# Kernel tuning notes

Hardware: AMD Instinct MI355X
Metric: run time of the kernel (lower is better)

The kernel has to match this reference:

```python
import jax, jax.numpy as jnp
import numpy as np

LSH_BUCKETS = 32
LSH_BANDWIDTH = 2.0
N_HASHES = 4
K_MAX = 64


def setup_inputs() -> dict:
    key0 = jax.random.key(0)
    kq, kk, kw = jax.random.split(key0, 3)
    B, L, D = 4, 4096, 64
    query = jax.random.normal(kq, (B, L, D), dtype=jnp.float32)
    key = jax.random.normal(kk, (B, L, D), dtype=jnp.float32)
    # learned LSH projection: maps binary features (D) -> N_HASHES hash values
    W = jax.random.normal(kw, (D, N_HASHES), dtype=jnp.float32)
    return {"query": query, "key": key, "W": W, "head_idx": 0}


def _lsh_hash(x_bin, W):
    # standard E2LSH-style hash: floor(<x, w> / bandwidth) mod n_buckets
    proj = x_bin @ W  # (B, L, N_HASHES)
    return jnp.floor(proj / LSH_BANDWIDTH).astype(jnp.int32) % LSH_BUCKETS


def reference(query, key, W, head_idx):
    B, L, _ = query.shape
    # binary_quantize: (x > 0).float()
    q_bin = (query > 0).astype(query.dtype)
    k_bin = (key > 0).astype(key.dtype)
    qh = _lsh_hash(q_bin, W)  # (B, L, N_HASHES) ints in [0, LSH_BUCKETS)
    kh = _lsh_hash(k_bin, W)
    # pack the N_HASHES hash values into one integer code per token;
    # codes equal  <=>  all hash values equal (values are in [0, LSH_BUCKETS))
    radix = (LSH_BUCKETS ** jnp.arange(N_HASHES)).astype(jnp.int32)  # (N_HASHES,)
    q_code = jnp.sum(qh * radix, axis=-1)  # (B, L)
    k_code = jnp.sum(kh * radix, axis=-1)  # (B, L)
    # match[b, i, j] = all hashes of query i equal hashes of key j
    match = q_code[:, :, None] == k_code[:, None, :]  # (B, L, L) bool
    # collect first K_MAX matching j per (b, i), pad with -1 (matches the
    # sequential early-break loop since j is scanned in increasing order)
    j_idx = jnp.arange(L, dtype=jnp.int32)
    score = jnp.where(match, j_idx[None, None, :], L)  # non-matches pushed to end
    first = jnp.sort(score, axis=-1)[:, :, :K_MAX]      # (B, L, K_MAX)
    candidates = jnp.where(first < L, first, -1)        # int32 indices, -1 pad
    return candidates
```

## Files before the change

kernel.cpp:

```cpp
#include <hip/hip_runtime.h>

#define KMAX 64
#define BB 4
#define LL 4096
#define DD 64
#define TOK (BB * LL)

typedef unsigned long long u64;

__global__ __launch_bounds__(64) void codes_kernel(
        const float* __restrict__ q,
        const float* __restrict__ k,
        const float* __restrict__ W,
        int* __restrict__ codes ) {
    __shared__ float sW[DD * 4];
    int lane = threadIdx.x;
    #pragma unroll
    for (int i = 0; i < 4; ++i) sW[i * 64 + lane] = W[i * 64 + lane];
    __syncthreads();

    int u = blockIdx.x * 64 + lane;
    const float* src = (u < TOK) ? q : k;
    int t = u & (TOK - 1);

    const float4* xp = (const float4*)(src + (size_t)t * DD);
    float4 x[16];
    #pragma unroll
    for (int i = 0; i < 16; ++i) x[i] = xp[i];

    float p0 = 0.f, p1 = 0.f, p2 = 0.f, p3 = 0.f;
    const float4* wrow = (const float4*)sW;
    #pragma unroll
    for (int d = 0; d < DD; ++d) {
        float xv = ((const float*)x)[d];
        float b = (xv > 0.f) ? 1.0f : 0.0f;
        float4 w = wrow[d];
        p0 = fmaf(b, w.x, p0);
        p1 = fmaf(b, w.y, p1);
        p2 = fmaf(b, w.z, p2);
        p3 = fmaf(b, w.w, p3);
    }
    int h0 = ((int)floorf(p0 * 0.5f)) & 31;
    int h1 = ((int)floorf(p1 * 0.5f)) & 31;
    int h2 = ((int)floorf(p2 * 0.5f)) & 31;
    int h3 = ((int)floorf(p3 * 0.5f)) & 31;
    codes[u] = h0 | (h1 << 5) | (h2 << 10) | (h3 << 15);
}

__global__ __launch_bounds__(256) void find_kernel(
        const int* __restrict__ qcodes,
        const int* __restrict__ kcodes,
        int* __restrict__ out) {
    int gtid = blockIdx.x * 256 + threadIdx.x;
    int wave = gtid >> 6;
    int lane = gtid & 63;
    int b = wave >> 12;
    int qc = qcodes[wave];
    const int4* kc4 = (const int4*)(kcodes + b * LL);
    int* op = out + (size_t)wave * KMAX;
    u64 lowmask = (1ull << lane) - 1ull;

    int count = 0;
    for (int g = 0; g < LL / 256 && count < KMAX; ++g) {
        int4 kv = kc4[g * 64 + lane];
        bool m0 = (kv.x == qc), m1 = (kv.y == qc);
        bool m2 = (kv.z == qc), m3 = (kv.w == qc);
        if (__ballot(m0 | m1 | m2 | m3) == 0) continue;
        u64 b0 = __ballot(m0), b1 = __ballot(m1);
        u64 b2 = __ballot(m2), b3 = __ballot(m3);
        int before = __popcll(b0 & lowmask) + __popcll(b1 & lowmask)
                   + __popcll(b2 & lowmask) + __popcll(b3 & lowmask);
        int pos = count + before;
        int j0 = g * 256 + lane * 4;
        if (m0) { if (pos < KMAX) op[pos] = j0;     ++pos; }
        if (m1) { if (pos < KMAX) op[pos] = j0 + 1; ++pos; }
        if (m2) { if (pos < KMAX) op[pos] = j0 + 2; ++pos; }
        if (m3) { if (pos < KMAX) op[pos] = j0 + 3; ++pos; }
        count += __popcll(b0) + __popcll(b1) + __popcll(b2) + __popcll(b3);
    }
    int p = count + lane;
    if (p < KMAX) op[p] = -1;
}

extern "C" void kernel_launch(void* const* d_in, const int* in_sizes, int n_in,
                              void* d_out, int out_size, void* d_ws, size_t ws_size,
                              hipStream_t stream) {
    const float* q = (const float*)d_in[0];
    const float* k = (const float*)d_in[1];
    const float* W = (const float*)d_in[2];
    int* out = (int*)d_out;
    int* codes = (int*)d_ws;
    int* qcodes = codes;
    int* kcodes = codes + TOK;

    codes_kernel<<<(2 * TOK) / 64, 64, 0, stream>>>(q, k, W, codes);

    const int total_threads = TOK * 64;
    find_kernel<<<total_threads / 256, 256, 0, stream>>>(qcodes, kcodes, out);
}
```

Baseline: 23.69 us.

## Fuse code hashing and candidate search into one cooperative kernel

```diff
diff --git a/kernel.cpp b/kernel.cpp
--- a/kernel.cpp
+++ b/kernel.cpp
@@ -1,33 +1,119 @@
 #include <hip/hip_runtime.h>
+#include <hip/hip_cooperative_groups.h>
+
+namespace cg = cooperative_groups;
 
 #define KMAX 64
 #define BB 4
 #define LL 4096
 #define DD 64
 #define TOK (BB * LL)
+#define NBLK 512
+#define QPW 8
 
 typedef unsigned long long u64;
+
+__global__ __launch_bounds__(256) void fused_kernel(
+        const float* __restrict__ q,
+        const float* __restrict__ k,
+        const float* __restrict__ W,
+        int* __restrict__ codes ,
+        int* __restrict__ out) {
+    __shared__ float sW[DD * 4];
+    int tid = threadIdx.x;
+    sW[tid] = W[tid];
+    __syncthreads();
+
+    int gt = blockIdx.x * 256 + tid;
+
+    if (gt < 2 * TOK) {
+        const float* src = (gt < TOK) ? q : k;
+        int t = gt & (TOK - 1);
+        const float4* xp = (const float4*)(src + (size_t)t * DD);
+        float4 x[16];
+        #pragma unroll
+        for (int i = 0; i < 16; ++i) x[i] = xp[i];
+
+        float p0 = 0.f, p1 = 0.f, p2 = 0.f, p3 = 0.f;
+        const float4* wrow = (const float4*)sW;
+        #pragma unroll
+        for (int d = 0; d < DD; ++d) {
+            float xv = ((const float*)x)[d];
+            float b = (xv > 0.f) ? 1.0f : 0.0f;
+            float4 w = wrow[d];
+            p0 = fmaf(b, w.x, p0);
+            p1 = fmaf(b, w.y, p1);
+            p2 = fmaf(b, w.z, p2);
+            p3 = fmaf(b, w.w, p3);
+        }
+        int h0 = ((int)floorf(p0 * 0.5f)) & 31;
+        int h1 = ((int)floorf(p1 * 0.5f)) & 31;
+        int h2 = ((int)floorf(p2 * 0.5f)) & 31;
+        int h3 = ((int)floorf(p3 * 0.5f)) & 31;
+        codes[gt] = h0 | (h1 << 5) | (h2 << 10) | (h3 << 15);
+    }
+
+    cg::this_grid().sync();
+
+    int lane = tid & 63;
+    int wv = gt >> 6;
+    int qbase = wv * QPW;
+    int b = qbase >> 12;
+    const int4* kc4 = (const int4*)(codes + TOK + b * LL);
+    const int* qp = codes + qbase;
+    int* outb = out + (size_t)qbase * KMAX;
+    u64 lowmask = (1ull << lane) - 1ull;
+
+    int qc[QPW], cnt[QPW];
+    #pragma unroll
+    for (int i = 0; i < QPW; ++i) { qc[i] = qp[i]; cnt[i] = 0; }
+
+    for (int g = 0; g < LL / 256; ++g) {
+        int4 kv = kc4[g * 64 + lane];
+        int j0 = g * 256 + lane * 4;
+        #pragma unroll
+        for (int i = 0; i < QPW; ++i) {
+            if (cnt[i] >= KMAX) continue;
+            bool m0 = (kv.x == qc[i]), m1 = (kv.y == qc[i]);
+            bool m2 = (kv.z == qc[i]), m3 = (kv.w == qc[i]);
+            if (__ballot(m0 | m1 | m2 | m3) == 0) continue;
+            u64 b0 = __ballot(m0), b1 = __ballot(m1);
+            u64 b2 = __ballot(m2), b3 = __ballot(m3);
+            int before = __popcll(b0 & lowmask) + __popcll(b1 & lowmask)
+                       + __popcll(b2 & lowmask) + __popcll(b3 & lowmask);
+            int pos = cnt[i] + before;
+            int* op = outb + i * KMAX;
+            if (m0) { if (pos < KMAX) op[pos] = j0;     ++pos; }
+            if (m1) { if (pos < KMAX) op[pos] = j0 + 1; ++pos; }
+            if (m2) { if (pos < KMAX) op[pos] = j0 + 2; ++pos; }
+            if (m3) { if (pos < KMAX) op[pos] = j0 + 3; ++pos; }
+            cnt[i] += __popcll(b0) + __popcll(b1) + __popcll(b2) + __popcll(b3);
+        }
+    }
+    #pragma unroll
+    for (int i = 0; i < QPW; ++i) {
+        int p = cnt[i] + lane;
+        if (p < KMAX) outb[i * KMAX + p] = -1;
+    }
+}
 
 __global__ __launch_bounds__(64) void codes_kernel(
         const float* __restrict__ q,
         const float* __restrict__ k,
         const float* __restrict__ W,
-        int* __restrict__ codes ) {
+        int* __restrict__ codes) {
     __shared__ float sW[DD * 4];
     int lane = threadIdx.x;
     #pragma unroll
     for (int i = 0; i < 4; ++i) sW[i * 64 + lane] = W[i * 64 + lane];
     __syncthreads();
-
     int u = blockIdx.x * 64 + lane;
     const float* src = (u < TOK) ? q : k;
     int t = u & (TOK - 1);
-
     const float4* xp = (const float4*)(src + (size_t)t * DD);
     float4 x[16];
     #pragma unroll
     for (int i = 0; i < 16; ++i) x[i] = xp[i];
-
     float p0 = 0.f, p1 = 0.f, p2 = 0.f, p3 = 0.f;
     const float4* wrow = (const float4*)sW;
     #pragma unroll
@@ -59,7 +145,6 @@
     const int4* kc4 = (const int4*)(kcodes + b * LL);
     int* op = out + (size_t)wave * KMAX;
     u64 lowmask = (1ull << lane) - 1ull;
-
     int count = 0;
     for (int g = 0; g < LL / 256 && count < KMAX; ++g) {
         int4 kv = kc4[g * 64 + lane];
@@ -90,11 +175,13 @@
     const float* W = (const float*)d_in[2];
     int* out = (int*)d_out;
     int* codes = (int*)d_ws;
-    int* qcodes = codes;
-    int* kcodes = codes + TOK;
 
-    codes_kernel<<<(2 * TOK) / 64, 64, 0, stream>>>(q, k, W, codes);
-
-    const int total_threads = TOK * 64;
-    find_kernel<<<total_threads / 256, 256, 0, stream>>>(qcodes, kcodes, out);
+    void* args[] = {(void*)&q, (void*)&k, (void*)&W, (void*)&codes, (void*)&out};
+    hipError_t e = hipLaunchCooperativeKernel((const void*)fused_kernel,
+                                              dim3(NBLK), dim3(256), args, 0, stream);
+    if (e != hipSuccess) {
+        (void)hipGetLastError();
+        codes_kernel<<<(2 * TOK) / 64, 64, 0, stream>>>(q, k, W, codes);
+        find_kernel<<<(TOK * 64) / 256, 256, 0, stream>>>(codes, codes + TOK, out);
+    }
 }
```

After: 73.85 us. +211.7%, slower.

## Process four queries per wavefront to reuse key code loads

Applied to the files above, without the earlier changes.

```diff
diff --git a/kernel.cpp b/kernel.cpp
--- a/kernel.cpp
+++ b/kernel.cpp
@@ -5,6 +5,7 @@
 #define LL 4096
 #define DD 64
 #define TOK (BB * LL)
+#define QPW 4
 
 typedef unsigned long long u64;
 
@@ -54,32 +55,49 @@
     int gtid = blockIdx.x * 256 + threadIdx.x;
     int wave = gtid >> 6;
     int lane = gtid & 63;
-    int b = wave >> 12;
-    int qc = qcodes[wave];
+    int qbase = wave * QPW;
+    int b = qbase >> 12;
     const int4* kc4 = (const int4*)(kcodes + b * LL);
-    int* op = out + (size_t)wave * KMAX;
+    const int* qp = qcodes + qbase;
+    int* outb = out + (size_t)qbase * KMAX;
     u64 lowmask = (1ull << lane) - 1ull;
 
-    int count = 0;
-    for (int g = 0; g < LL / 256 && count < KMAX; ++g) {
+    int qc[QPW], cnt[QPW];
+    #pragma unroll
+    for (int i = 0; i < QPW; ++i) { qc[i] = qp[i]; cnt[i] = 0; }
+
+    for (int g = 0; g < LL / 256; ++g) {
         int4 kv = kc4[g * 64 + lane];
-        bool m0 = (kv.x == qc), m1 = (kv.y == qc);
-        bool m2 = (kv.z == qc), m3 = (kv.w == qc);
-        if (__ballot(m0 | m1 | m2 | m3) == 0) continue;
-        u64 b0 = __ballot(m0), b1 = __ballot(m1);
-        u64 b2 = __ballot(m2), b3 = __ballot(m3);
-        int before = __popcll(b0 & lowmask) + __popcll(b1 & lowmask)
-                   + __popcll(b2 & lowmask) + __popcll(b3 & lowmask);
-        int pos = count + before;
+        bool a0 = (kv.x == qc[0]) | (kv.y == qc[0]) | (kv.z == qc[0]) | (kv.w == qc[0]);
+        bool a1 = (kv.x == qc[1]) | (kv.y == qc[1]) | (kv.z == qc[1]) | (kv.w == qc[1]);
+        bool a2 = (kv.x == qc[2]) | (kv.y == qc[2]) | (kv.z == qc[2]) | (kv.w == qc[2]);
+        bool a3 = (kv.x == qc[3]) | (kv.y == qc[3]) | (kv.z == qc[3]) | (kv.w == qc[3]);
+        if (__ballot(a0 | a1 | a2 | a3) == 0) continue;
         int j0 = g * 256 + lane * 4;
-        if (m0) { if (pos < KMAX) op[pos] = j0;     ++pos; }
-        if (m1) { if (pos < KMAX) op[pos] = j0 + 1; ++pos; }
-        if (m2) { if (pos < KMAX) op[pos] = j0 + 2; ++pos; }
-        if (m3) { if (pos < KMAX) op[pos] = j0 + 3; ++pos; }
-        count += __popcll(b0) + __popcll(b1) + __popcll(b2) + __popcll(b3);
+        #pragma unroll
+        for (int i = 0; i < QPW; ++i) {
+            if (cnt[i] >= KMAX) continue;
+            bool m0 = (kv.x == qc[i]), m1 = (kv.y == qc[i]);
+            bool m2 = (kv.z == qc[i]), m3 = (kv.w == qc[i]);
+            if (__ballot(m0 | m1 | m2 | m3) == 0) continue;
+            u64 b0 = __ballot(m0), b1 = __ballot(m1);
+            u64 b2 = __ballot(m2), b3 = __ballot(m3);
+            int before = __popcll(b0 & lowmask) + __popcll(b1 & lowmask)
+                       + __popcll(b2 & lowmask) + __popcll(b3 & lowmask);
+            int pos = cnt[i] + before;
+            int* op = outb + i * KMAX;
+            if (m0) { if (pos < KMAX) op[pos] = j0;     ++pos; }
+            if (m1) { if (pos < KMAX) op[pos] = j0 + 1; ++pos; }
+            if (m2) { if (pos < KMAX) op[pos] = j0 + 2; ++pos; }
+            if (m3) { if (pos < KMAX) op[pos] = j0 + 3; ++pos; }
+            cnt[i] += __popcll(b0) + __popcll(b1) + __popcll(b2) + __popcll(b3);
+        }
     }
-    int p = count + lane;
-    if (p < KMAX) op[p] = -1;
+    #pragma unroll
+    for (int i = 0; i < QPW; ++i) {
+        int p = cnt[i] + lane;
+        if (p < KMAX) outb[i * KMAX + p] = -1;
+    }
 }
 
 extern "C" void kernel_launch(void* const* d_in, const int* in_sizes, int n_in,
@@ -95,6 +113,6 @@
 
     codes_kernel<<<(2 * TOK) / 64, 64, 0, stream>>>(q, k, W, codes);
 
-    const int total_threads = TOK * 64;
+    const int total_threads = (TOK / QPW) * 64;
     find_kernel<<<total_threads / 256, 256, 0, stream>>>(qcodes, kcodes, out);
 }
```

New measurement: 21.13 us. -10.8%, faster.
